# Kernel tuning notes

Hardware: AMD Instinct MI355X
Metric: run time of the kernel (lower is better)

The kernel has to match this reference:

```python
import jax, jax.numpy as jnp
import numpy as np

N = 20000      # num nodes
E = 320000     # num edges
F_IN = 512
HEADS = 8
D = 64         # out_features per head (512 / 8)
ALPHA = 0.2    # leaky relu slope
EPS = 1e-16


def setup_inputs() -> dict:
    key = jax.random.key(0)
    k1, k2, k3, k4, k5 = jax.random.split(key, 5)
    x = jax.random.normal(k1, (N, F_IN), dtype=jnp.float32)
    edge_index = jax.random.randint(k2, (2, E), 0, N, dtype=jnp.int64)
    # per-head parameters (xavier-normal-ish scale)
    s_w = np.sqrt(2.0 / (F_IN + D))
    W_e = jax.random.normal(k3, (HEADS, F_IN, D), dtype=jnp.float32) * s_w
    W_r = jax.random.normal(k4, (HEADS, F_IN, D), dtype=jnp.float32) * s_w
    # attention vector over concat of [h_src, h_dst, diff, |diff|, prod] -> 5*D
    s_a = np.sqrt(2.0 / (1 + 5 * D))
    a = jax.random.normal(k5, (HEADS, 5 * D), dtype=jnp.float32) * s_a
    return {"x": x, "edge_index": edge_index, "W_e": W_e, "W_r": W_r, "a": a}


def _gat_forward(x, edge_index, W_e, W_r, a):
    src = edge_index[0]  # [E] softmax / output rows
    dst = edge_index[1]  # [E]

    h_e = jnp.einsum('nf,hfd->hnd', x, W_e)  # [H,N,D]
    h_r = jnp.einsum('nf,hfd->hnd', x, W_r)  # [H,N,D]

    a_src, a_dst, a_dif, a_abs, a_prd = jnp.split(a, 5, axis=1)  # each [H,D]

    # node-level dot products for the linear concat parts, then gather
    s_src = jnp.einsum('hnd,hd->hn', h_e, a_src)[:, src]  # [H,E]
    s_dst = jnp.einsum('hnd,hd->hn', h_e, a_dst)[:, dst]  # [H,E]

    hr_src = h_r[:, src]            # [H,E,D]
    hr_dst = h_r[:, dst]            # [H,E,D]
    diff = hr_dst - hr_src          # [H,E,D]
    score = (s_src + s_dst
             + jnp.einsum('hed,hd->he', diff, a_dif)
             + jnp.einsum('hed,hd->he', jnp.abs(diff), a_abs)
             + jnp.einsum('hed,hd->he', hr_src * hr_dst, a_prd))  # [H,E]

    alpha = jax.nn.leaky_relu(score, negative_slope=ALPHA)  # [H,E]

    # sparse softmax over edges grouped by source node
    alpha_t = alpha.T  # [E,H]
    m = jax.ops.segment_max(alpha_t, src, num_segments=N)        # [N,H]
    ex = jnp.exp(alpha_t - m[src])                                # [E,H]
    denom = jax.ops.segment_sum(ex, src, num_segments=N)[src]    # [E,H]
    att = ex / (denom + EPS)                                      # [E,H]

    # spmm: out[src] += att * h_e[dst]
    msg = att[:, :, None] * jnp.transpose(h_e[:, dst], (1, 0, 2))  # [E,H,D]
    out = jax.ops.segment_sum(msg, src, num_segments=N)            # [N,H,D]
    return out.reshape(N, HEADS * D)  # concat heads along feature dim


def reference(x, edge_index, W_e, W_r, a):
    return _gat_forward(x, edge_index, W_e, W_r, a)
```

## Files before the change

### kernel.cpp

```cpp
#include <hip/hip_runtime.h>
#include <hip/hip_bf16.h>

#define N_NODES 20000
#define N_EDGES 320000
#define F_IN 512
#define HEADS 8
#define DH 64

typedef __attribute__((ext_vector_type(8))) short short8;
typedef __attribute__((ext_vector_type(4))) float f32x4;

__device__ inline short f2bf(float f) {
  __hip_bfloat16 h = __float2bfloat16(f);
  return __builtin_bit_cast(short, h);
}
__device__ inline void unpack8(short8 s, float f[8]) {
  uint4 u = __builtin_bit_cast(uint4, s);
  f[0] = __builtin_bit_cast(float, u.x << 16);
  f[1] = __builtin_bit_cast(float, u.x & 0xFFFF0000u);
  f[2] = __builtin_bit_cast(float, u.y << 16);
  f[3] = __builtin_bit_cast(float, u.y & 0xFFFF0000u);
  f[4] = __builtin_bit_cast(float, u.z << 16);
  f[5] = __builtin_bit_cast(float, u.z & 0xFFFF0000u);
  f[6] = __builtin_bit_cast(float, u.w << 16);
  f[7] = __builtin_bit_cast(float, u.w & 0xFFFF0000u);
}
__device__ __forceinline__ void async_copy16(void* lds_base, const void* g) {
  __builtin_amdgcn_global_load_lds(
      (const __attribute__((address_space(1))) unsigned int*)g,
      (__attribute__((address_space(3))) unsigned int*)lds_base, 16, 0, 0);
}

__global__ __launch_bounds__(256) void cast_x_kernel(
    const float* __restrict__ x, short* __restrict__ xb)
{
  int i = (blockIdx.x * 256 + threadIdx.x) * 4;
  if (i < N_NODES * F_IN) {
    float4 v = *(const float4*)&x[i];
    short4 o;
    o.x = f2bf(v.x); o.y = f2bf(v.y); o.z = f2bf(v.z); o.w = f2bf(v.w);
    *(short4*)&xb[i] = o;
  }
}

__global__ __launch_bounds__(256) void cast_w_kernel(
    const float* __restrict__ We, const float* __restrict__ Wr, short* __restrict__ Wt)
{
  __shared__ short tile[64 * 65];
  const int b = blockIdx.x;
  const int kt = (b & 7) * 64;
  const int h = (b >> 3) & 7;
  const int mat = b >> 6;
  const float* __restrict__ W = (mat ? Wr : We) + (size_t)h * F_IN * DH;
  #pragma unroll
  for (int r = 0; r < 16; ++r) {
    int idx = r * 256 + threadIdx.x;
    int k = idx >> 6, d = idx & 63;
    tile[d * 65 + k] = f2bf(W[(size_t)(kt + k) * DH + d]);
  }
  __syncthreads();
  short* __restrict__ Wo = Wt + (size_t)(mat * 8 + h) * 64 * F_IN;
  #pragma unroll
  for (int r = 0; r < 16; ++r) {
    int idx = r * 256 + threadIdx.x;
    int d = idx >> 6, k = idx & 63;
    Wo[(size_t)d * F_IN + kt + k] = tile[d * 65 + k];
  }
}

#define GBM 128
#define GBN 128
#define GBK 64
#define MT_TOTAL 157
#define MT_PER_GRP 20

__global__ __launch_bounds__(256) void gemm_mfma(
    const short* __restrict__ xb, const short* __restrict__ Wt,
    short* __restrict__ he, short* __restrict__ hr,
    const float* __restrict__ a,
    float* __restrict__ ssrc, float* __restrict__ sdst)
{
  const int b = blockIdx.x;
  const int g = b & 7;
  const int j = b >> 3;
  const int m_tile = g * MT_PER_GRP + (j >> 3);
  const int c_tile = j & 7;
  if (m_tile >= MT_TOTAL) return;

  __shared__ short As[GBM * GBK];
  __shared__ short Bs[GBN * GBK];
  const int tid = threadIdx.x;
  const int m0 = m_tile * GBM;
  const int n0 = c_tile * GBN;
  const int wv = tid >> 6, lane = tid & 63, quad = lane >> 4, l16 = lane & 15;
  const int wm = (wv >> 1) * 64;
  const int wn = (wv & 1) * 64;
  const int lrow = lane >> 3;
  const int gc = (lane & 7) ^ (lrow & 7);

  f32x4 acc[4][4] = {};

  for (int kt = 0; kt < F_IN; kt += GBK) {
    #pragma unroll
    for (int s = 0; s < 4; ++s) {
      int seg = wv * 4 + s;
      int row = seg * 8 + lrow;
      async_copy16(&As[seg * 512],
                   &xb[(size_t)(m0 + row) * F_IN + kt + gc * 8]);
      async_copy16(&Bs[seg * 512],
                   &Wt[(size_t)(n0 + row) * F_IN + kt + gc * 8]);
    }
    __syncthreads();
    #pragma unroll
    for (int ks = 0; ks < 2; ++ks) {
      short8 af[4], bf4[4];
      const int ch = ((ks << 2) + quad) ^ (l16 & 7);
      #pragma unroll
      for (int i = 0; i < 4; ++i)
        af[i] = *(const short8*)&As[(wm + i * 16 + l16) * GBK + ch * 8];
      #pragma unroll
      for (int jj = 0; jj < 4; ++jj)
        bf4[jj] = *(const short8*)&Bs[(wn + jj * 16 + l16) * GBK + ch * 8];
      #pragma unroll
      for (int i = 0; i < 4; ++i)
        #pragma unroll
        for (int jj = 0; jj < 4; ++jj)
          acc[i][jj] = __builtin_amdgcn_mfma_f32_16x16x32_bf16(af[i], bf4[jj], acc[i][jj], 0, 0, 0);
    }
    __syncthreads();
  }

  const int cb = c_tile * 2 + (wv & 1);
  const int mat = cb >> 3, h = cb & 7;
  short* __restrict__ C = mat ? hr : he;
  #pragma unroll
  for (int i = 0; i < 4; ++i) {
    #pragma unroll
    for (int r = 0; r < 4; ++r) {
      int m = m0 + wm + i * 16 + quad * 4 + r;
      if (m < N_NODES) {
        #pragma unroll
        for (int jj = 0; jj < 4; ++jj)
          C[((size_t)m * HEADS + h) * DH + jj * 16 + l16] = f2bf(acc[i][jj][r]);
      }
    }
  }

  if (mat == 0) {
    float as4[4], ad4[4];
    #pragma unroll
    for (int jj = 0; jj < 4; ++jj) {
      as4[jj] = a[h * 320 + jj * 16 + l16];
      ad4[jj] = a[h * 320 + 64 + jj * 16 + l16];
    }
    #pragma unroll
    for (int i = 0; i < 4; ++i) {
      #pragma unroll
      for (int r = 0; r < 4; ++r) {
        int m = m0 + wm + i * 16 + quad * 4 + r;
        float v1 = 0.f, v2 = 0.f;
        #pragma unroll
        for (int jj = 0; jj < 4; ++jj) {
          v1 = fmaf(acc[i][jj][r], as4[jj], v1);
          v2 = fmaf(acc[i][jj][r], ad4[jj], v2);
        }
        #pragma unroll
        for (int s = 1; s < 16; s <<= 1) {
          v1 += __shfl_xor(v1, s);
          v2 += __shfl_xor(v2, s);
        }
        if (l16 == 0 && m < N_NODES) {
          ssrc[(size_t)m * HEADS + h] = v1;
          sdst[(size_t)m * HEADS + h] = v2;
        }
      }
    }
  }
}

__global__ void hist_kernel(const int* __restrict__ ei, int* __restrict__ deg) {
  int e = blockIdx.x * blockDim.x + threadIdx.x;
  if (e < N_EDGES) atomicAdd(&deg[ei[e]], 1);
}

#define SC_NB 20

__global__ __launch_bounds__(1024) void scan_pre(
    const int* __restrict__ deg, int* __restrict__ bsum)
{
  __shared__ int wsum[16];
  int tid = threadIdx.x, wv = tid >> 6, ln = tid & 63;
  int i = blockIdx.x * 1024 + tid;
  int v = (i < N_NODES) ? deg[i] : 0;
  #pragma unroll
  for (int d = 32; d >= 1; d >>= 1) v += __shfl_xor(v, d);
  if (ln == 0) wsum[wv] = v;
  __syncthreads();
  if (tid == 0) {
    int s = 0;
    #pragma unroll
    for (int k = 0; k < 16; ++k) s += wsum[k];
    bsum[blockIdx.x] = s;
  }
}

__global__ void scan_mid(const int* __restrict__ bsum, int* __restrict__ bbase,
                         int* __restrict__ off)
{
  int ln = threadIdx.x;
  int v = (ln < SC_NB) ? bsum[ln] : 0;
  int s = v;
  #pragma unroll
  for (int d = 1; d < 64; d <<= 1) {
    int t = __shfl_up(s, d);
    if (ln >= d) s += t;
  }
  if (ln < SC_NB) bbase[ln] = s - v;
  if (ln == SC_NB - 1) off[N_NODES] = s;
}

__global__ __launch_bounds__(1024) void scan_fin(
    const int* __restrict__ deg, const int* __restrict__ bbase, int* __restrict__ off)
{
  __shared__ int wsum[16];
  int tid = threadIdx.x, wv = tid >> 6, ln = tid & 63;
  int i = blockIdx.x * 1024 + tid;
  int v = (i < N_NODES) ? deg[i] : 0;
  int s = v;
  #pragma unroll
  for (int d = 1; d < 64; d <<= 1) {
    int t = __shfl_up(s, d);
    if (ln >= d) s += t;
  }
  if (ln == 63) wsum[wv] = s;
  __syncthreads();
  if (wv == 0 && ln < 16) {
    int t = wsum[ln];
    #pragma unroll
    for (int d = 1; d < 16; d <<= 1) {
      int u = __shfl_up(t, d);
      if (ln >= d) t += u;
    }
    wsum[ln] = t;
  }
  __syncthreads();
  int base = bbase[blockIdx.x] + (wv ? wsum[wv - 1] : 0);
  if (i < N_NODES) off[i] = base + s - v;
}

__global__ void scatter_kernel(const int* __restrict__ ei, const int* __restrict__ off,
                               int* __restrict__ cnt, int* __restrict__ csr_dst) {
  int e = blockIdx.x * blockDim.x + threadIdx.x;
  if (e < N_EDGES) {
    int s = ei[e];
    int t = ei[N_EDGES + e];
    int pos = off[s] + atomicAdd(&cnt[s], 1);
    csr_dst[pos] = t;
  }
}

__global__ __launch_bounds__(256) void attn_kernel(
    const short* __restrict__ he, const short* __restrict__ hr,
    const float* __restrict__ a, const float* __restrict__ ssrc,
    const float* __restrict__ sdst, const int* __restrict__ off,
    const int* __restrict__ csr_dst, float* __restrict__ out)
{
  const int wv = threadIdx.x >> 6;
  const int n = blockIdx.x * 4 + wv;
  const int lane = threadIdx.x & 63;
  const int h = lane >> 3;
  const int d0 = (lane & 7) * 8;
  const int beg = off[n], end = off[n + 1];

  float hrn[8];
  unpack8(*(const short8*)&hr[(size_t)n * 512 + lane * 8], hrn);
  float adif[8], aabs[8], aprd[8];
  const int ab = h * 320;
  *(float4*)&adif[0] = *(const float4*)&a[ab + 128 + d0];
  *(float4*)&adif[4] = *(const float4*)&a[ab + 128 + d0 + 4];
  *(float4*)&aabs[0] = *(const float4*)&a[ab + 192 + d0];
  *(float4*)&aabs[4] = *(const float4*)&a[ab + 192 + d0 + 4];
  *(float4*)&aprd[0] = *(const float4*)&a[ab + 256 + d0];
  *(float4*)&aprd[4] = *(const float4*)&a[ab + 256 + d0 + 4];
  const float sbase = ssrc[(size_t)n * HEADS + h];

  float denom = 0.f;
  float acc[8] = {};

  auto process = [&](int t) {
    short8 hr8 = *(const short8*)&hr[(size_t)t * 512 + lane * 8];
    short8 he8 = *(const short8*)&he[(size_t)t * 512 + lane * 8];
    float sd = sdst[(size_t)t * HEADS + h];
    float hrd[8], hed[8];
    unpack8(hr8, hrd);
    unpack8(he8, hed);
    float v = 0.f;
    #pragma unroll
    for (int j = 0; j < 8; ++j) {
      float df = hrd[j] - hrn[j];
      v = fmaf(df, adif[j], v);
      v = fmaf(fabsf(df), aabs[j], v);
      v = fmaf(hrn[j] * hrd[j], aprd[j], v);
    }
    v += __shfl_xor(v, 1);
    v += __shfl_xor(v, 2);
    v += __shfl_xor(v, 4);
    float sc = sbase + sd + v;
    sc = fmaxf(sc, 0.2f * sc);
    float ex = __expf(sc);
    denom += ex;
    #pragma unroll
    for (int j = 0; j < 8; ++j) acc[j] = fmaf(ex, hed[j], acc[j]);
  };

  int i = beg;
  for (; i + 1 < end; i += 2) {
    int t0 = csr_dst[i], t1 = csr_dst[i + 1];
    process(t0);
    process(t1);
  }
  if (i < end) process(csr_dst[i]);

  float inv = 1.f / (denom + 1e-16f);
  float4 o0, o1;
  o0.x = acc[0] * inv; o0.y = acc[1] * inv; o0.z = acc[2] * inv; o0.w = acc[3] * inv;
  o1.x = acc[4] * inv; o1.y = acc[5] * inv; o1.z = acc[6] * inv; o1.w = acc[7] * inv;
  *(float4*)&out[(size_t)n * 512 + lane * 8] = o0;
  *(float4*)&out[(size_t)n * 512 + lane * 8 + 4] = o1;
}

extern "C" void kernel_launch(void* const* d_in, const int* in_sizes, int n_in,
                              void* d_out, int out_size, void* d_ws, size_t ws_size,
                              hipStream_t stream) {
  const float* x  = (const float*)d_in[0];
  const int*   ei = (const int*)d_in[1];
  const float* We = (const float*)d_in[2];
  const float* Wr = (const float*)d_in[3];
  const float* a  = (const float*)d_in[4];
  float* out = (float*)d_out;

  char* ws = (char*)d_ws;
  size_t p = 0;
  auto alloc = [&](size_t bytes) {
    void* r = ws + p;
    p = (p + bytes + 255) & ~(size_t)255;
    return r;
  };
  short* xb = (short*)alloc(sizeof(short) * (size_t)N_NODES * F_IN);
  short* Wt = (short*)alloc(sizeof(short) * 2 * HEADS * F_IN * DH);
  short* he = (short*)alloc(sizeof(short) * (size_t)N_NODES * HEADS * DH);
  short* hr = (short*)alloc(sizeof(short) * (size_t)N_NODES * HEADS * DH);
  float* ssrc = (float*)alloc(sizeof(float) * (size_t)N_NODES * HEADS);
  float* sdst = (float*)alloc(sizeof(float) * (size_t)N_NODES * HEADS);
  int* degcnt = (int*)alloc(sizeof(int) * 2 * N_NODES);
  int* deg = degcnt;
  int* cnt = degcnt + N_NODES;
  int* off = (int*)alloc(sizeof(int) * (N_NODES + 1));
  int* csr = (int*)alloc(sizeof(int) * N_EDGES);
  int* bsum = (int*)alloc(sizeof(int) * SC_NB);
  int* bbase = (int*)alloc(sizeof(int) * SC_NB);

  hipMemsetAsync(degcnt, 0, sizeof(int) * 2 * N_NODES, stream);

  cast_x_kernel<<<(N_NODES * F_IN / 4 + 255) / 256, 256, 0, stream>>>(x, xb);
  cast_w_kernel<<<128, 256, 0, stream>>>(We, Wr, Wt);

  gemm_mfma<<<8 * MT_PER_GRP * 8, 256, 0, stream>>>(xb, Wt, he, hr, a, ssrc, sdst);

  hist_kernel<<<(N_EDGES + 255) / 256, 256, 0, stream>>>(ei, deg);
  scan_pre<<<SC_NB, 1024, 0, stream>>>(deg, bsum);
  scan_mid<<<1, 64, 0, stream>>>(bsum, bbase, off);
  scan_fin<<<SC_NB, 1024, 0, stream>>>(deg, bbase, off);
  scatter_kernel<<<(N_EDGES + 255) / 256, 256, 0, stream>>>(ei, off, cnt, csr);
  attn_kernel<<<N_NODES / 4, 256, 0, stream>>>(he, hr, a, ssrc, sdst, off, csr, out);
}
```

Measured before the change: 274.4 us.

## Fuse prologue kernels, double-buffer GEMM LDS, batch edge gathers in attention

```diff
diff --git a/kernel.cpp b/kernel.cpp
--- a/kernel.cpp
+++ b/kernel.cpp
@@ -31,40 +31,46 @@
       (__attribute__((address_space(3))) unsigned int*)lds_base, 16, 0, 0);
 }
 
-__global__ __launch_bounds__(256) void cast_x_kernel(
-    const float* __restrict__ x, short* __restrict__ xb)
-{
-  int i = (blockIdx.x * 256 + threadIdx.x) * 4;
-  if (i < N_NODES * F_IN) {
+#define CX_BLOCKS 10000
+#define CW_BLOCKS 128
+#define HI_BLOCKS 1250
+
+__global__ __launch_bounds__(256) void prologue_kernel(
+    const float* __restrict__ x, const float* __restrict__ We,
+    const float* __restrict__ Wr, const int* __restrict__ ei,
+    short* __restrict__ xb, short* __restrict__ Wt, int* __restrict__ deg)
+{
+  __shared__ short tile[64 * 65];
+  const int b = blockIdx.x;
+  if (b < CX_BLOCKS) {
+    int i = (b * 256 + threadIdx.x) * 4;
     float4 v = *(const float4*)&x[i];
     short4 o;
     o.x = f2bf(v.x); o.y = f2bf(v.y); o.z = f2bf(v.z); o.w = f2bf(v.w);
     *(short4*)&xb[i] = o;
-  }
-}
-
-__global__ __launch_bounds__(256) void cast_w_kernel(
-    const float* __restrict__ We, const float* __restrict__ Wr, short* __restrict__ Wt)
-{
-  __shared__ short tile[64 * 65];
-  const int b = blockIdx.x;
-  const int kt = (b & 7) * 64;
-  const int h = (b >> 3) & 7;
-  const int mat = b >> 6;
-  const float* __restrict__ W = (mat ? Wr : We) + (size_t)h * F_IN * DH;
-  #pragma unroll
-  for (int r = 0; r < 16; ++r) {
-    int idx = r * 256 + threadIdx.x;
-    int k = idx >> 6, d = idx & 63;
-    tile[d * 65 + k] = f2bf(W[(size_t)(kt + k) * DH + d]);
-  }
-  __syncthreads();
-  short* __restrict__ Wo = Wt + (size_t)(mat * 8 + h) * 64 * F_IN;
-  #pragma unroll
-  for (int r = 0; r < 16; ++r) {
-    int idx = r * 256 + threadIdx.x;
-    int d = idx >> 6, k = idx & 63;
-    Wo[(size_t)d * F_IN + kt + k] = tile[d * 65 + k];
+  } else if (b < CX_BLOCKS + CW_BLOCKS) {
+    const int bb = b - CX_BLOCKS;
+    const int kt = (bb & 7) * 64;
+    const int h = (bb >> 3) & 7;
+    const int mat = bb >> 6;
+    const float* __restrict__ W = (mat ? Wr : We) + (size_t)h * F_IN * DH;
+    #pragma unroll
+    for (int r = 0; r < 16; ++r) {
+      int idx = r * 256 + threadIdx.x;
+      int k = idx >> 6, d = idx & 63;
+      tile[d * 65 + k] = f2bf(W[(size_t)(kt + k) * DH + d]);
+    }
+    __syncthreads();
+    short* __restrict__ Wo = Wt + (size_t)(mat * 8 + h) * 64 * F_IN;
+    #pragma unroll
+    for (int r = 0; r < 16; ++r) {
+      int idx = r * 256 + threadIdx.x;
+      int d = idx >> 6, k = idx & 63;
+      Wo[(size_t)d * F_IN + kt + k] = tile[d * 65 + k];
+    }
+  } else {
+    int e = (b - CX_BLOCKS - CW_BLOCKS) * 256 + threadIdx.x;
+    if (e < N_EDGES) atomicAdd(&deg[ei[e]], 1);
   }
 }
 
@@ -73,6 +79,7 @@
 #define GBK 64
 #define MT_TOTAL 157
 #define MT_PER_GRP 20
+#define NKT (F_IN / GBK)
 
 __global__ __launch_bounds__(256) void gemm_mfma(
     const short* __restrict__ xb, const short* __restrict__ Wt,
@@ -87,8 +94,8 @@
   const int c_tile = j & 7;
   if (m_tile >= MT_TOTAL) return;
 
-  __shared__ short As[GBM * GBK];
-  __shared__ short Bs[GBN * GBK];
+  __shared__ short As[2][GBM * GBK];
+  __shared__ short Bs[2][GBN * GBK];
   const int tid = threadIdx.x;
   const int m0 = m_tile * GBM;
   const int n0 = c_tile * GBN;
@@ -100,27 +107,34 @@
 
   f32x4 acc[4][4] = {};
 
-  for (int kt = 0; kt < F_IN; kt += GBK) {
+  auto stage = [&](int kt, int buf) {
     #pragma unroll
     for (int s = 0; s < 4; ++s) {
       int seg = wv * 4 + s;
       int row = seg * 8 + lrow;
-      async_copy16(&As[seg * 512],
+      async_copy16(&As[buf][seg * 512],
                    &xb[(size_t)(m0 + row) * F_IN + kt + gc * 8]);
-      async_copy16(&Bs[seg * 512],
+      async_copy16(&Bs[buf][seg * 512],
                    &Wt[(size_t)(n0 + row) * F_IN + kt + gc * 8]);
     }
-    __syncthreads();
+  };
+
+  stage(0, 0);
+  __syncthreads();
+  for (int it = 0; it < NKT; ++it) {
+    if (it + 1 < NKT) stage((it + 1) * GBK, (it + 1) & 1);
+    const short* __restrict__ Ab = &As[it & 1][0];
+    const short* __restrict__ Bb = &Bs[it & 1][0];
     #pragma unroll
     for (int ks = 0; ks < 2; ++ks) {
       short8 af[4], bf4[4];
       const int ch = ((ks << 2) + quad) ^ (l16 & 7);
       #pragma unroll
       for (int i = 0; i < 4; ++i)
-        af[i] = *(const short8*)&As[(wm + i * 16 + l16) * GBK + ch * 8];
+        af[i] = *(const short8*)&Ab[(wm + i * 16 + l16) * GBK + ch * 8];
       #pragma unroll
       for (int jj = 0; jj < 4; ++jj)
-        bf4[jj] = *(const short8*)&Bs[(wn + jj * 16 + l16) * GBK + ch * 8];
+        bf4[jj] = *(const short8*)&Bb[(wn + jj * 16 + l16) * GBK + ch * 8];
       #pragma unroll
       for (int i = 0; i < 4; ++i)
         #pragma unroll
@@ -178,11 +192,6 @@
   }
 }
 
-__global__ void hist_kernel(const int* __restrict__ ei, int* __restrict__ deg) {
-  int e = blockIdx.x * blockDim.x + threadIdx.x;
-  if (e < N_EDGES) atomicAdd(&deg[ei[e]], 1);
-}
-
 #define SC_NB 20
 
 __global__ __launch_bounds__(1024) void scan_pre(
@@ -287,20 +296,17 @@
   float denom = 0.f;
   float acc[8] = {};
 
-  auto process = [&](int t) {
-    short8 hr8 = *(const short8*)&hr[(size_t)t * 512 + lane * 8];
-    short8 he8 = *(const short8*)&he[(size_t)t * 512 + lane * 8];
-    float sd = sdst[(size_t)t * HEADS + h];
+  auto edge = [&](short8 hr8, short8 he8, float sd) {
     float hrd[8], hed[8];
     unpack8(hr8, hrd);
     unpack8(he8, hed);
     float v = 0.f;
     #pragma unroll
-    for (int j = 0; j < 8; ++j) {
-      float df = hrd[j] - hrn[j];
-      v = fmaf(df, adif[j], v);
-      v = fmaf(fabsf(df), aabs[j], v);
-      v = fmaf(hrn[j] * hrd[j], aprd[j], v);
+    for (int jj = 0; jj < 8; ++jj) {
+      float df = hrd[jj] - hrn[jj];
+      v = fmaf(df, adif[jj], v);
+      v = fmaf(fabsf(df), aabs[jj], v);
+      v = fmaf(hrn[jj] * hrd[jj], aprd[jj], v);
     }
     v += __shfl_xor(v, 1);
     v += __shfl_xor(v, 2);
@@ -310,16 +316,36 @@
     float ex = __expf(sc);
     denom += ex;
     #pragma unroll
-    for (int j = 0; j < 8; ++j) acc[j] = fmaf(ex, hed[j], acc[j]);
+    for (int jj = 0; jj < 8; ++jj) acc[jj] = fmaf(ex, hed[jj], acc[jj]);
   };
 
   int i = beg;
-  for (; i + 1 < end; i += 2) {
-    int t0 = csr_dst[i], t1 = csr_dst[i + 1];
-    process(t0);
-    process(t1);
-  }
-  if (i < end) process(csr_dst[i]);
+  for (; i + 4 <= end; i += 4) {
+    int t0 = csr_dst[i], t1 = csr_dst[i + 1], t2 = csr_dst[i + 2], t3 = csr_dst[i + 3];
+    short8 r0 = *(const short8*)&hr[(size_t)t0 * 512 + lane * 8];
+    short8 e0 = *(const short8*)&he[(size_t)t0 * 512 + lane * 8];
+    short8 r1 = *(const short8*)&hr[(size_t)t1 * 512 + lane * 8];
+    short8 e1 = *(const short8*)&he[(size_t)t1 * 512 + lane * 8];
+    short8 r2 = *(const short8*)&hr[(size_t)t2 * 512 + lane * 8];
+    short8 e2 = *(const short8*)&he[(size_t)t2 * 512 + lane * 8];
+    short8 r3 = *(const short8*)&hr[(size_t)t3 * 512 + lane * 8];
+    short8 e3 = *(const short8*)&he[(size_t)t3 * 512 + lane * 8];
+    float s0 = sdst[(size_t)t0 * HEADS + h];
+    float s1 = sdst[(size_t)t1 * HEADS + h];
+    float s2 = sdst[(size_t)t2 * HEADS + h];
+    float s3 = sdst[(size_t)t3 * HEADS + h];
+    edge(r0, e0, s0);
+    edge(r1, e1, s1);
+    edge(r2, e2, s2);
+    edge(r3, e3, s3);
+  }
+  for (; i < end; ++i) {
+    int t = csr_dst[i];
+    short8 r0 = *(const short8*)&hr[(size_t)t * 512 + lane * 8];
+    short8 e0 = *(const short8*)&he[(size_t)t * 512 + lane * 8];
+    float s0 = sdst[(size_t)t * HEADS + h];
+    edge(r0, e0, s0);
+  }
 
   float inv = 1.f / (denom + 1e-16f);
   float4 o0, o1;
@@ -362,12 +388,11 @@
 
   hipMemsetAsync(degcnt, 0, sizeof(int) * 2 * N_NODES, stream);
 
-  cast_x_kernel<<<(N_NODES * F_IN / 4 + 255) / 256, 256, 0, stream>>>(x, xb);
-  cast_w_kernel<<<128, 256, 0, stream>>>(We, Wr, Wt);
+  prologue_kernel<<<CX_BLOCKS + CW_BLOCKS + HI_BLOCKS, 256, 0, stream>>>(
+      x, We, Wr, ei, xb, Wt, deg);
 
   gemm_mfma<<<8 * MT_PER_GRP * 8, 256, 0, stream>>>(xb, Wt, he, hr, a, ssrc, sdst);
 
-  hist_kernel<<<(N_EDGES + 255) / 256, 256, 0, stream>>>(ei, deg);
   scan_pre<<<SC_NB, 1024, 0, stream>>>(deg, bsum);
   scan_mid<<<1, 64, 0, stream>>>(bsum, bbase, off);
   scan_fin<<<SC_NB, 1024, 0, stream>>>(deg, bbase, off);
```

After: 268.3 us. -2.2%, faster.
